# Kernel tuning notes

Hardware: AMD Instinct MI355X
Metric: run time of the kernel (lower is better)

Reference implementation:

```python
import jax, jax.numpy as jnp
import numpy as np

N_UNI = 32; N_G = 4; N_PPG = 8
MAX_D = 100.0; MIN_D = 0.5
SOM_SIGMA = 2.0; G_STD = 2.5
ORIG = jnp.array([-25.6, -25.6, -2.0], jnp.float32); VS = 0.4
NZ = 16; GW = 128; GL = 128; DIM = 128
H_IMG = 352; W_IMG = 1216

def pe(x):
    # positional encoding: num_freqs=6, include_input -> 3 + 36 = 39 dims
    f = 2.0 ** jnp.arange(6, dtype=x.dtype)
    xf = x[..., None] * f  # (...,3,6)
    s = x.shape[:-1]
    return jnp.concatenate([x, jnp.sin(xf).reshape(s + (18,)), jnp.cos(xf).reshape(s + (18,))], axis=-1)

def resnet_fc(z, x, P):
    # pixelNeRF-style ResnetFC with latent injection per block
    w_in, b_in, wz, bz, w0, b0, w1, b1, w_out, b_out = P
    h = x @ w_in + b_in
    for i in range(3):
        h = h + z @ wz[i] + bz[i]
        net = jax.nn.relu(h) @ w0[i] + b0[i]
        h = h + jax.nn.relu(net) @ w1[i] + b1[i]
    return jax.nn.relu(h) @ w_out + b_out

def trilinear(grid, pts):
    # grid: (NZ,GW,GL,DIM); pts: (N,3) lidar coords -> trilinear gather, 0 outside
    g = (pts - ORIG) / VS
    gx, gy, gz = g[:, 0], g[:, 1], g[:, 2]
    inb = (gx >= 0) & (gx <= GW - 1) & (gy >= 0) & (gy <= GL - 1) & (gz >= 0) & (gz <= NZ - 1)
    gx = jnp.clip(gx, 0.0, GW - 1.0); gy = jnp.clip(gy, 0.0, GL - 1.0); gz = jnp.clip(gz, 0.0, NZ - 1.0)
    x0 = jnp.clip(jnp.floor(gx).astype(jnp.int32), 0, GW - 2)
    y0 = jnp.clip(jnp.floor(gy).astype(jnp.int32), 0, GL - 2)
    z0 = jnp.clip(jnp.floor(gz).astype(jnp.int32), 0, NZ - 2)
    fx = gx - x0; fy = gy - y0; fz = gz - z0
    def c(zi, xi, yi, w):
        return grid[zi, xi, yi] * w[:, None]
    feat = (c(z0, x0, y0, (1 - fz) * (1 - fx) * (1 - fy)) + c(z0, x0, y0 + 1, (1 - fz) * (1 - fx) * fy)
            + c(z0, x0 + 1, y0, (1 - fz) * fx * (1 - fy)) + c(z0, x0 + 1, y0 + 1, (1 - fz) * fx * fy)
            + c(z0 + 1, x0, y0, fz * (1 - fx) * (1 - fy)) + c(z0 + 1, x0, y0 + 1, fz * (1 - fx) * fy)
            + c(z0 + 1, x0 + 1, y0, fz * fx * (1 - fy)) + c(z0 + 1, x0 + 1, y0 + 1, fz * fx * fy))
    return feat * inb[:, None].astype(feat.dtype)

def bilinear(img, uv):
    # img: (3,H,W); uv: (N,2) (u=col, v=row) -> (N,3)
    _, H, W = img.shape
    u = jnp.clip(uv[:, 0], 0.0, W - 1.0); v = jnp.clip(uv[:, 1], 0.0, H - 1.0)
    u0 = jnp.clip(jnp.floor(u).astype(jnp.int32), 0, W - 2)
    v0 = jnp.clip(jnp.floor(v).astype(jnp.int32), 0, H - 2)
    fu = u - u0; fv = v - v0
    g = lambda vi, ui: img[:, vi, ui]
    out = (g(v0, u0) * ((1 - fv) * (1 - fu)) + g(v0, u0 + 1) * ((1 - fv) * fu)
           + g(v0 + 1, u0) * (fv * (1 - fu)) + g(v0 + 1, u0 + 1) * (fv * fu))
    return out.T

def _forward(bev_feature, cam_K, img_source, img_target, T_source2infer, T_source2target,
             gaussian_noise, Pm, Pg, sampled_pixels):
    R = sampled_pixels.shape[0]
    # (B, C, W, L) -> (n_z, W, L, dim)
    vf = bev_feature[0].reshape(NZ, DIM, GW, GL).transpose(0, 2, 3, 1)
    inv_K = jnp.linalg.inv(cam_K)
    pix = sampled_pixels.astype(jnp.float32)
    homog = jnp.concatenate([pix, jnp.ones((R, 1), jnp.float32)], axis=1)
    dirs = homog @ inv_K.T
    unit = dirs / jnp.linalg.norm(dirs, axis=1, keepdims=True)  # (R,3) cam frame
    Rsi = T_source2infer[:3, :3]; tsi = T_source2infer[:3, 3]
    viewdir = unit @ Rsi.T  # lidar frame

    # --- predict per-ray gaussian means/stds at coarse segment centers ---
    base = (jnp.arange(N_G, dtype=jnp.float32) + 0.5) * (MAX_D / N_G)
    pg = (unit[:, None, :] * base[None, :, None]).reshape(-1, 3) @ Rsi.T + tsi
    fg = trilinear(vf, pg)
    vdg = jnp.broadcast_to(viewdir[:, None, :], (R, N_G, 3)).reshape(-1, 3)
    og = resnet_fc(fg, jnp.concatenate([pe(pg), vdg], axis=1), Pg)  # (R*N_G,2)
    means = jnp.clip(base[None, :] + og[:, 0].reshape(R, N_G), MIN_D, MAX_D)
    stds = G_STD * jax.nn.sigmoid(og[:, 1].reshape(R, N_G)) + 0.1

    # --- sample points: uniform + gaussian, sorted along ray ---
    d_g = jnp.clip(means[:, :, None] + stds[:, :, None] * gaussian_noise, MIN_D, MAX_D).reshape(R, N_G * N_PPG)
    d_u = jnp.broadcast_to(jnp.linspace(MIN_D, MAX_D, N_UNI, dtype=jnp.float32)[None, :], (R, N_UNI))
    d = jnp.sort(jnp.concatenate([d_u, d_g], axis=1), axis=1)  # (R,64)
    P = d.shape[1]
    pl = (unit[:, None, :] * d[..., None]).reshape(-1, 3) @ Rsi.T + tsi
    fl = trilinear(vf, pl)
    vd = jnp.broadcast_to(viewdir[:, None, :], (R, P, 3)).reshape(-1, 3)
    out = resnet_fc(fl, jnp.concatenate([pe(pl), vd], axis=1), Pm).reshape(R, P, 4)
    sigma = jax.nn.softplus(out[..., 0]); rgb = jax.nn.sigmoid(out[..., 1:])

    # --- volume rendering ---
    deltas = jnp.concatenate([d[:, 1:] - d[:, :-1], jnp.full((R, 1), 1e10, jnp.float32)], axis=1)
    alpha = 1.0 - jnp.exp(-sigma * deltas)
    trans = jnp.cumprod(1.0 - alpha + 1e-10, axis=1)
    trans = jnp.concatenate([jnp.ones((R, 1), jnp.float32), trans[:, :-1]], axis=1)
    w = alpha * trans
    depth = (w * d).sum(axis=1)          # (R,)
    color = (w[..., None] * rgb).sum(axis=1)  # (R,3)

    # --- losses ---
    diff = jnp.abs(means - jax.lax.stop_gradient(depth)[:, None])
    loss_dist = diff.min(axis=1)
    pdf = jnp.exp(-(d[:, None, :] - means[..., None]) ** 2 / (2.0 * stds[..., None] ** 2)) / (stds[..., None] * jnp.sqrt(2.0 * jnp.pi))
    loss_kl = (w * (-jnp.log(pdf.mean(axis=1) + 1e-6))).sum(axis=1)
    src = bilinear(img_source, pix)
    loss_color = jnp.abs(src - color)
    pcam = unit * depth[:, None]
    pt = pcam @ T_source2target[:3, :3].T + T_source2target[:3, 3]
    proj = pt @ cam_K.T
    uv = proj[:, :2] / jnp.clip(proj[:, 2:3], 1e-3)
    tgt = bilinear(img_target, uv)
    loss_reproj = jnp.abs(src - tgt)
    total = loss_reproj.mean() + loss_color.mean() + loss_kl.mean() + 0.01 * loss_dist.mean()
    return total

def setup_inputs() -> dict:
    key = jax.random.key(0)
    def rn(i, shape, s=1.0):
        return jax.random.normal(jax.random.fold_in(key, i), shape, jnp.float32) * s
    R = 4096
    inp = {}
    inp['bev_feature'] = rn(0, (1, NZ * DIM, GW, GL), 0.5)
    inp['cam_K'] = jnp.array([[720.0, 0.0, 608.0], [0.0, 720.0, 176.0], [0.0, 0.0, 1.0]], jnp.float32)
    inp['img_source'] = jax.random.uniform(jax.random.fold_in(key, 1), (3, H_IMG, W_IMG), jnp.float32)
    inp['img_target'] = jax.random.uniform(jax.random.fold_in(key, 2), (3, H_IMG, W_IMG), jnp.float32)
    Rcl = jnp.array([[0.0, 0.0, 1.0], [-1.0, 0.0, 0.0], [0.0, -1.0, 0.0]], jnp.float32)  # cam->lidar axes
    inp['T_source2infer'] = jnp.eye(4, dtype=jnp.float32).at[:3, :3].set(Rcl).at[:3, 3].set(jnp.array([0.5, 0.2, 0.1], jnp.float32))
    inp['T_source2target'] = jnp.eye(4, dtype=jnp.float32).at[0, 3].set(0.8).at[1, 3].set(0.05)
    inp['gaussian_noise'] = rn(3, (R, N_G, N_PPG))
    u = jax.random.randint(jax.random.fold_in(key, 4), (R,), 0, W_IMG)
    v = jax.random.randint(jax.random.fold_in(key, 5), (R,), 0, H_IMG)
    inp['sampled_pixels'] = jnp.stack([u, v], axis=1).astype(jnp.int32)
    for pfx, (i0, d_out) in {'m': (10, 4), 'g': (40, 2)}.items():
        inp[pfx + '_w_in'] = rn(i0, (42, 128), 0.05)
        inp[pfx + '_b_in'] = jnp.zeros((128,), jnp.float32)
        inp[pfx + '_wz'] = rn(i0 + 1, (3, 128, 128), 0.05)
        inp[pfx + '_bz'] = jnp.zeros((3, 128), jnp.float32)
        inp[pfx + '_w0'] = rn(i0 + 2, (3, 128, 128), 0.05)
        inp[pfx + '_b0'] = jnp.zeros((3, 128), jnp.float32)
        inp[pfx + '_w1'] = rn(i0 + 3, (3, 128, 128), 0.05)
        inp[pfx + '_b1'] = jnp.zeros((3, 128), jnp.float32)
        inp[pfx + '_w_out'] = rn(i0 + 4, (128, d_out), 0.05)
        inp[pfx + '_b_out'] = jnp.zeros((d_out,), jnp.float32)
    return inp

def reference(bev_feature, cam_K, img_source, img_target, T_source2infer, T_source2target,
              gaussian_noise, sampled_pixels,
              m_w_in, m_b_in, m_wz, m_bz, m_w0, m_b0, m_w1, m_b1, m_w_out, m_b_out,
              g_w_in, g_b_in, g_wz, g_bz, g_w0, g_b0, g_w1, g_b1, g_w_out, g_b_out):
    Pm = (m_w_in, m_b_in, m_wz, m_bz, m_w0, m_b0, m_w1, m_b1, m_w_out, m_b_out)
    Pg = (g_w_in, g_b_in, g_wz, g_bz, g_w0, g_b0, g_w1, g_b1, g_w_out, g_b_out)
    return _forward(bev_feature, cam_K, img_source, img_target, T_source2infer, T_source2target,
                    gaussian_noise, Pm, Pg, sampled_pixels)
```

## Files before the change

kernel.cpp:

```cpp
#include <hip/hip_runtime.h>

typedef __attribute__((ext_vector_type(8))) short short8;
typedef __attribute__((ext_vector_type(4))) float f32x4;
typedef unsigned short ushort_t;

#define WIMG 1216
#define HIMG 352

__device__ __forceinline__ float sigmoid_(float x){ return 1.f/(1.f+__expf(-x)); }
__device__ __forceinline__ float softplus_(float x){
  return fmaxf(x,0.f) + log1pf(__expf(-fabsf(x)));
}
__device__ __forceinline__ ushort_t f2b(float x){
  union { float f; unsigned u; } v; v.f = x;
  unsigned r = v.u + 0x7FFF + ((v.u >> 16) & 1);
  return (ushort_t)(r >> 16);
}
__device__ __forceinline__ ushort_t f2b_fast(float x){
  union { float f; unsigned u; } v; v.f = x;
  return (ushort_t)((v.u + 0x8000u) >> 16);
}
__device__ __forceinline__ unsigned pack2bf(float a, float b){
  union { float f; unsigned u; } va, vb; va.f = a; vb.f = b;
  return ((va.u + 0x8000u) >> 16) | ((vb.u + 0x8000u) & 0xFFFF0000u);
}
__device__ __forceinline__ float b2f(ushort_t b){
  union { unsigned u; float f; } v; v.u = ((unsigned)b) << 16;
  return v.f;
}
__device__ __forceinline__ float b2f_lo(unsigned u){
  union { unsigned u; float f; } v; v.u = u << 16; return v.f;
}
__device__ __forceinline__ float b2f_hi(unsigned u){
  union { unsigned u; float f; } v; v.u = u & 0xFFFF0000u; return v.f;
}

__global__ void k_pack(const float* __restrict__ w_in, const float* __restrict__ wz,
                       const float* __restrict__ w0, const float* __restrict__ w1,
                       const float* __restrict__ w_out, int outd,
                       ushort_t* __restrict__ pk){
  int id = blockIdx.x*256 + threadIdx.x;
  if (id >= 39*4096) return;
  int blk = id >> 12;
  int e = id & 4095;
  float val = 0.f;
  if (blk < 38) {
    int nt = e >> 9, lane = (e >> 3) & 63, j = e & 7;
    int kloc = (lane >> 4)*8 + j;
    int n = nt*16 + (lane & 15);
    if (blk < 2) {
      int k = blk*32 + kloc;
      val = (k < 42) ? w_in[k*128 + n] : 0.f;
    } else {
      int g = blk - 2;
      int i = g / 12, r = g % 12, m = r >> 2, ks = r & 3;
      int k = ks*32 + kloc;
      const float* src = (m==0 ? wz : (m==1 ? w0 : w1)) + i*16384;
      val = src[k*128 + n];
    }
  } else if (e < 2048) {
    int ks = e >> 9, lane = (e >> 3) & 63, j = e & 7;
    int k = ks*32 + (lane >> 4)*8 + j;
    int n = lane & 15;
    val = (n < outd) ? w_out[k*outd + n] : 0.f;
  }
  pk[id] = f2b(val);
}

__global__ void k_transpose(const float* __restrict__ src, ushort_t* __restrict__ dst){
  __shared__ float tile[32][33];
  int zx = blockIdx.z;
  int y0 = blockIdx.x * 32;
  int c0 = blockIdx.y * 32;
  int z = zx >> 7, x = zx & 127;
  const float* s = src + (size_t)z*2097152 + (size_t)x*128;
  for (int i = threadIdx.y; i < 32; i += 8)
    tile[i][threadIdx.x] = s[(size_t)(c0+i)*16384 + (size_t)(y0 + threadIdx.x)];
  __syncthreads();
  ushort_t* d = dst + ((size_t)zx*128 + y0)*128 + c0;
  int idx = threadIdx.y*32 + threadIdx.x;
  for (int it = 0; it < 2; ++it) {
    int lin = it*256 + idx;
    int y = lin >> 4, cp = lin & 15;
    unsigned o = pack2bf(tile[cp*2][y], tile[cp*2+1][y]);
    *(unsigned*)(d + (size_t)y*128 + cp*2) = o;
  }
}

__global__ void k_rayinit(const float* __restrict__ camK, const int* __restrict__ pix,
                          const float* __restrict__ Tsi,
                          float* __restrict__ unit, float* __restrict__ viewdir, int R){
  int r = blockIdx.x*blockDim.x + threadIdx.x;
  if (r >= R) return;
  float a=camK[0],b=camK[1],c=camK[2],d=camK[3],e=camK[4],f=camK[5],g=camK[6],h=camK[7],i=camK[8];
  float c00 = e*i-f*h, c01 = c*h-b*i, c02 = b*f-c*e;
  float c10 = f*g-d*i, c11 = a*i-c*g, c12 = c*d-a*f;
  float c20 = d*h-e*g, c21 = b*g-a*h, c22 = a*e-b*d;
  float det = a*c00 + b*c10 + c*c20;
  float id = 1.f/det;
  float u = (float)pix[2*r], v = (float)pix[2*r+1];
  float dx = (c00*u + c01*v + c02)*id;
  float dy = (c10*u + c11*v + c12)*id;
  float dz = (c20*u + c21*v + c22)*id;
  float n = sqrtf(dx*dx+dy*dy+dz*dz);
  dx/=n; dy/=n; dz/=n;
  unit[3*r]=dx; unit[3*r+1]=dy; unit[3*r+2]=dz;
  viewdir[3*r]   = Tsi[0]*dx + Tsi[1]*dy + Tsi[2]*dz;
  viewdir[3*r+1] = Tsi[4]*dx + Tsi[5]*dy + Tsi[6]*dz;
  viewdir[3*r+2] = Tsi[8]*dx + Tsi[9]*dy + Tsi[10]*dz;
}

template<int KS>
__device__ __forceinline__ void gemm_acc(const ushort_t* lds, int pitch,
                                         const ushort_t* __restrict__ pkB,
                                         f32x4 acc[4][2], int wave, int lane)
{
  int l15 = lane & 15, quad = lane >> 4;
  short8 b[2*KS];
  #pragma unroll
  for (int ks = 0; ks < KS; ++ks)
    #pragma unroll
    for (int ct = 0; ct < 2; ++ct)
      b[ks*2+ct] = *(const short8*)(pkB + (size_t)((ks*8 + wave*2 + ct)*64 + lane)*8);
  #pragma unroll
  for (int ks = 0; ks < KS; ++ks) {
    short8 a[4];
    #pragma unroll
    for (int rt = 0; rt < 4; ++rt)
      a[rt] = *(const short8*)(lds + (rt*16 + l15)*pitch + ks*32 + quad*8);
    #pragma unroll
    for (int rt = 0; rt < 4; ++rt)
      #pragma unroll
      for (int ct = 0; ct < 2; ++ct)
        acc[rt][ct] = __builtin_amdgcn_mfma_f32_16x16x32_bf16(a[rt], b[ks*2+ct], acc[rt][ct], 0,0,0);
  }
}

__device__ __forceinline__ void store_relu(ushort_t* buf, const f32x4 acc[4][2], int wave, int lane){
  int l15 = lane & 15, quad = lane >> 4;
  #pragma unroll
  for (int rt = 0; rt < 4; ++rt)
    #pragma unroll
    for (int ct = 0; ct < 2; ++ct) {
      int n = (wave*2+ct)*16 + l15;
      #pragma unroll
      for (int r = 0; r < 4; ++r) {
        int p = rt*16 + quad*4 + r;
        buf[p*136 + n] = f2b_fast(fmaxf(acc[rt][ct][r], 0.f));
      }
    }
}

template<int OUTD, int RAY_SHIFT>
__global__ __launch_bounds__(256, 4)
void k_fused(const ushort_t* __restrict__ vfh, const float* __restrict__ vf0, int mode,
             const float* __restrict__ unit, const float* __restrict__ viewdir,
             const float* __restrict__ Tsi, const float* __restrict__ dvals,
             const ushort_t* __restrict__ pk,
             const float* __restrict__ b_in, const float* __restrict__ bzv,
             const float* __restrict__ b0v, const float* __restrict__ b1v,
             const float* __restrict__ b_out,
             float* __restrict__ means, float* __restrict__ stds, float* __restrict__ outbuf)
{
  __shared__ int   sOff[64];
  __shared__ float sFx[64], sFy[64], sFz[64], sSc[64];
  __shared__ float sPx[64], sPy[64], sPz[64], sVx[64], sVy[64], sVz[64];
  __shared__ ushort_t zf[64*136];
  __shared__ ushort_t Wb[64*136];

  int tid = threadIdx.x;
  int qbase = blockIdx.x * 64;

  if (tid < 64) {
    int q = qbase + tid;
    int ray = q >> RAY_SHIFT;
    float t;
    if constexpr (OUTD == 2) t = ((float)(q & 3) + 0.5f) * 25.f;
    else                     t = dvals[q];
    float ux = unit[3*ray], uy = unit[3*ray+1], uz = unit[3*ray+2];
    float wx=ux*t, wy=uy*t, wz=uz*t;
    float px = Tsi[0]*wx + Tsi[1]*wy + Tsi[2]*wz + Tsi[3];
    float py = Tsi[4]*wx + Tsi[5]*wy + Tsi[6]*wz + Tsi[7];
    float pz = Tsi[8]*wx + Tsi[9]*wy + Tsi[10]*wz + Tsi[11];
    sPx[tid]=px; sPy[tid]=py; sPz[tid]=pz;
    sVx[tid]=viewdir[3*ray]; sVy[tid]=viewdir[3*ray+1]; sVz[tid]=viewdir[3*ray+2];
    float gx = (px + 25.6f)*2.5f;
    float gy = (py + 25.6f)*2.5f;
    float gz = (pz + 2.0f)*2.5f;
    bool inb = (gx>=0.f)&&(gx<=127.f)&&(gy>=0.f)&&(gy<=127.f)&&(gz>=0.f)&&(gz<=15.f);
    gx = fminf(fmaxf(gx,0.f),127.f);
    gy = fminf(fmaxf(gy,0.f),127.f);
    gz = fminf(fmaxf(gz,0.f),15.f);
    int x0 = min(max((int)floorf(gx),0),126);
    int y0 = min(max((int)floorf(gy),0),126);
    int z0 = min(max((int)floorf(gz),0),14);
    sFx[tid]=gx-(float)x0; sFy[tid]=gy-(float)y0; sFz[tid]=gz-(float)z0;
    sSc[tid]= inb ? 1.f : 0.f;
    sOff[tid] = mode ? (((z0*128 + x0)*128 + y0)*128)
                     : (z0*2097152 + x0*128 + y0);
  }
  __syncthreads();

  for (int it = 0; it < 16; ++it) {
    int lin = it*256 + tid;
    int p = lin >> 6, cp = lin & 63, c = cp*2;
    float fx=sFx[p], fy=sFy[p], fz=sFz[p], sc=sSc[p];
    float w000=(1.f-fz)*(1.f-fx)*(1.f-fy), w001=(1.f-fz)*(1.f-fx)*fy;
    float w010=(1.f-fz)*fx*(1.f-fy),       w011=(1.f-fz)*fx*fy;
    float w100=fz*(1.f-fx)*(1.f-fy),       w101=fz*(1.f-fx)*fy;
    float w110=fz*fx*(1.f-fy),             w111=fz*fx*fy;
    float r0, r1;
    if (mode) {
      const ushort_t* b = vfh + sOff[p] + c;
      unsigned v000 = *(const unsigned*)(b);
      unsigned v001 = *(const unsigned*)(b + 128);
      unsigned v010 = *(const unsigned*)(b + 16384);
      unsigned v011 = *(const unsigned*)(b + 16384 + 128);
      unsigned v100 = *(const unsigned*)(b + 2097152);
      unsigned v101 = *(const unsigned*)(b + 2097152 + 128);
      unsigned v110 = *(const unsigned*)(b + 2097152 + 16384);
      unsigned v111 = *(const unsigned*)(b + 2097152 + 16384 + 128);
      r0 = (w000*b2f_lo(v000) + w001*b2f_lo(v001) + w010*b2f_lo(v010) + w011*b2f_lo(v011)
          + w100*b2f_lo(v100) + w101*b2f_lo(v101) + w110*b2f_lo(v110) + w111*b2f_lo(v111)) * sc;
      r1 = (w000*b2f_hi(v000) + w001*b2f_hi(v001) + w010*b2f_hi(v010) + w011*b2f_hi(v011)
          + w100*b2f_hi(v100) + w101*b2f_hi(v101) + w110*b2f_hi(v110) + w111*b2f_hi(v111)) * sc;
    } else {
      const float* b = vf0 + sOff[p] + c*16384;
      r0 = (w000*b[0] + w001*b[1] + w010*b[128] + w011*b[129]
          + w100*b[2097152] + w101*b[2097153] + w110*b[2097280] + w111*b[2097281]) * sc;
      const float* b2 = b + 16384;
      r1 = (w000*b2[0] + w001*b2[1] + w010*b2[128] + w011*b2[129]
          + w100*b2[2097152] + w101*b2[2097153] + w110*b2[2097280] + w111*b2[2097281]) * sc;
    }
    *(unsigned*)(zf + p*136 + c) = pack2bf(r0, r1);
  }

  for (int it = 0; it < 16; ++it) {
    int lin = it*256 + tid;
    int p = lin >> 6, d = lin & 63;
    float val = 0.f;
    if (d < 3)      val = (d==0)?sPx[p]:((d==1)?sPy[p]:sPz[p]);
    else if (d < 39) {
      int s = d - 3; bool isSin = (s < 18); if (!isSin) s -= 18;
      int axis = s/6, fi = s%6;
      float base = (axis==0)?sPx[p]:((axis==1)?sPy[p]:sPz[p]);
      float arg = base * (float)(1 << fi);
      val = isSin ? __sinf(arg) : __cosf(arg);
    } else if (d < 42) {
      val = (d==39)?sVx[p]:((d==40)?sVy[p]:sVz[p]);
    }
    Wb[p*72 + d] = f2b_fast(val);
  }
  __syncthreads();

  int wave = tid >> 6, lane = tid & 63;
  int l15 = lane & 15, quad = lane >> 4;
  int n0 = (wave*2)*16 + l15;

  f32x4 h[4][2];
  {
    float bi0 = b_in[n0], bi1 = b_in[n0+16];
    #pragma unroll
    for (int rt = 0; rt < 4; ++rt) {
      h[rt][0] = (f32x4){bi0,bi0,bi0,bi0};
      h[rt][1] = (f32x4){bi1,bi1,bi1,bi1};
    }
  }
  gemm_acc<2>(Wb, 72, pk, h, wave, lane);

  const ushort_t* pkl = pk + 2*4096;
  #pragma unroll 1
  for (int i = 0; i < 3; ++i) {
    gemm_acc<4>(zf, 136, pkl + (size_t)(i*12)*4096, h, wave, lane);
    {
      float z0b = bzv[i*128 + n0], z1b = bzv[i*128 + n0 + 16];
      #pragma unroll
      for (int rt = 0; rt < 4; ++rt) { h[rt][0] += z0b; h[rt][1] += z1b; }
    }
    __syncthreads();
    store_relu(Wb, h, wave, lane);
    __syncthreads();
    f32x4 net[4][2];
    {
      float c0b = b0v[i*128 + n0], c1b = b0v[i*128 + n0 + 16];
      #pragma unroll
      for (int rt = 0; rt < 4; ++rt) {
        net[rt][0] = (f32x4){c0b,c0b,c0b,c0b};
        net[rt][1] = (f32x4){c1b,c1b,c1b,c1b};
      }
    }
    gemm_acc<4>(Wb, 136, pkl + (size_t)(i*12+4)*4096, net, wave, lane);
    __syncthreads();
    store_relu(Wb, net, wave, lane);
    __syncthreads();
    gemm_acc<4>(Wb, 136, pkl + (size_t)(i*12+8)*4096, h, wave, lane);
    {
      float o0b = b1v[i*128 + n0], o1b = b1v[i*128 + n0 + 16];
      #pragma unroll
      for (int rt = 0; rt < 4; ++rt) { h[rt][0] += o0b; h[rt][1] += o1b; }
    }
  }
  __syncthreads();
  store_relu(Wb, h, wave, lane);
  __syncthreads();

  {
    const ushort_t* pkw = pk + 38*4096;
    float bj = (l15 < OUTD) ? b_out[l15] : 0.f;
    f32x4 oa = (f32x4){bj,bj,bj,bj};
    #pragma unroll
    for (int ks = 0; ks < 4; ++ks) {
      short8 a = *(const short8*)(Wb + (wave*16 + l15)*136 + ks*32 + quad*8);
      short8 b = *(const short8*)(pkw + (size_t)(ks*64 + lane)*8);
      oa = __builtin_amdgcn_mfma_f32_16x16x32_bf16(a, b, oa, 0,0,0);
    }
    if (l15 < OUTD) {
      #pragma unroll
      for (int r = 0; r < 4; ++r) {
        int p = wave*16 + quad*4 + r;
        int q = qbase + p;
        if constexpr (OUTD == 4) {
          outbuf[(size_t)q*4 + l15] = oa[r];
        } else {
          int ray = q >> 2, g = q & 3;
          if (l15 == 0) means[ray*4+g] = fminf(fmaxf(((float)g + 0.5f)*25.f + oa[r], 0.5f), 100.f);
          else          stds[ray*4+g]  = 2.5f*sigmoid_(oa[r]) + 0.1f;
        }
      }
    }
  }
}

__global__ void k_sortd(const float* __restrict__ means, const float* __restrict__ stds,
                        const float* __restrict__ noise, float* __restrict__ dsort, int R){
  __shared__ float buf[4][64];
  int lr = threadIdx.x >> 6, p = threadIdx.x & 63;
  int ray = blockIdx.x*4 + lr;
  float val;
  if (p < 32) val = 0.5f + (float)p * (99.5f/31.f);
  else {
    int idx = p - 32, g = idx >> 3, s = idx & 7;
    float mu = means[ray*4+g], sd = stds[ray*4+g];
    val = fminf(fmaxf(mu + sd*noise[(ray*4+g)*8 + s], 0.5f), 100.f);
  }
  buf[lr][p] = val;
  __syncthreads();
  int rank = 0;
  for (int k = 0; k < 64; ++k) {
    float o = buf[lr][k];
    rank += (o < val) || (o == val && k < p);
  }
  dsort[ray*64 + rank] = val;
}

__device__ __forceinline__ void bilin3(const float* __restrict__ img, float u, float v, float* out){
  u = fminf(fmaxf(u, 0.f), (float)(WIMG-1));
  v = fminf(fmaxf(v, 0.f), (float)(HIMG-1));
  int u0 = min(max((int)floorf(u),0), WIMG-2);
  int v0 = min(max((int)floorf(v),0), HIMG-2);
  float fu = u - (float)u0, fv = v - (float)v0;
  float w00=(1.f-fv)*(1.f-fu), w01=(1.f-fv)*fu, w10=fv*(1.f-fu), w11=fv*fu;
  #pragma unroll
  for (int c = 0; c < 3; ++c) {
    const float* b = img + (size_t)c*(HIMG*WIMG) + (size_t)v0*WIMG + u0;
    out[c] = w00*b[0] + w01*b[1] + w10*b[WIMG] + w11*b[WIMG+1];
  }
}

__global__ void k_render(const float* __restrict__ outbuf, const float* __restrict__ dsort,
                         const float* __restrict__ means, const float* __restrict__ stds,
                         const float* __restrict__ unit,
                         const float* __restrict__ img_src, const float* __restrict__ img_tgt,
                         const int* __restrict__ pix, const float* __restrict__ camK,
                         const float* __restrict__ Tst, float* __restrict__ rayloss, int R){
  int gid = blockIdx.x*blockDim.x + threadIdx.x;
  int r = gid >> 6, lane = gid & 63;
  if (r >= R) return;
  float d = dsort[(size_t)r*64 + lane];
  float dn = __shfl_down(d, 1);
  float delta = (lane < 63) ? (dn - d) : 1e10f;
  float4 o = *(const float4*)(outbuf + (size_t)r*256 + lane*4);
  float sig = softplus_(o.x);
  float alpha = 1.f - __expf(-sig*delta);
  float om = 1.f - alpha + 1e-10f;
  float prod = om;
  #pragma unroll
  for (int off = 1; off < 64; off <<= 1) {
    float v = __shfl_up(prod, off);
    if (lane >= off) prod *= v;
  }
  float texc = __shfl_up(prod, 1);
  if (lane == 0) texc = 1.f;
  float w = alpha * texc;
  float m0=means[r*4],m1=means[r*4+1],m2=means[r*4+2],m3=means[r*4+3];
  float s0=stds[r*4], s1=stds[r*4+1], s2=stds[r*4+2], s3=stds[r*4+3];
  float t0=(d-m0)/s0, t1=(d-m1)/s1, t2=(d-m2)/s2, t3=(d-m3)/s3;
  float pm = 0.25f*0.3989422804014327f*(__expf(-0.5f*t0*t0)/s0 + __expf(-0.5f*t1*t1)/s1
                                      + __expf(-0.5f*t2*t2)/s2 + __expf(-0.5f*t3*t3)/s3);
  float kl  = w * (-__logf(pm + 1e-6f));
  float dep = w * d;
  float c0 = w * sigmoid_(o.y);
  float c1 = w * sigmoid_(o.z);
  float c2 = w * sigmoid_(o.w);
  #pragma unroll
  for (int off = 32; off; off >>= 1) {
    dep += __shfl_xor(dep, off);
    c0  += __shfl_xor(c0, off);
    c1  += __shfl_xor(c1, off);
    c2  += __shfl_xor(c2, off);
    kl  += __shfl_xor(kl, off);
  }
  if (lane == 0) {
    float ld = fminf(fminf(fabsf(m0-dep),fabsf(m1-dep)), fminf(fabsf(m2-dep),fabsf(m3-dep)));
    float src[3], tgt[3];
    float u = (float)pix[2*r], v = (float)pix[2*r+1];
    bilin3(img_src, u, v, src);
    float ux=unit[3*r],uy=unit[3*r+1],uz=unit[3*r+2];
    float pcx=ux*dep, pcy=uy*dep, pcz=uz*dep;
    float ptx = Tst[0]*pcx + Tst[1]*pcy + Tst[2]*pcz + Tst[3];
    float pty = Tst[4]*pcx + Tst[5]*pcy + Tst[6]*pcz + Tst[7];
    float ptz = Tst[8]*pcx + Tst[9]*pcy + Tst[10]*pcz + Tst[11];
    float prx = camK[0]*ptx + camK[1]*pty + camK[2]*ptz;
    float pry = camK[3]*ptx + camK[4]*pty + camK[5]*ptz;
    float prz = camK[6]*ptx + camK[7]*pty + camK[8]*ptz;
    prz = fmaxf(prz, 0.001f);
    bilin3(img_tgt, prx/prz, pry/prz, tgt);
    float lrepr = fabsf(src[0]-tgt[0])+fabsf(src[1]-tgt[1])+fabsf(src[2]-tgt[2]);
    float lcol  = fabsf(src[0]-c0)+fabsf(src[1]-c1)+fabsf(src[2]-c2);
    float invR = 1.f/(float)R;
    rayloss[r] = (lrepr + lcol) * (invR/3.f) + kl*invR + 0.01f*ld*invR;
  }
}

__global__ void k_reduce(const float* __restrict__ rayloss, float* __restrict__ out, int R){
  __shared__ float sm[256];
  float acc = 0.f;
  for (int i = threadIdx.x; i < R; i += 256) acc += rayloss[i];
  sm[threadIdx.x] = acc;
  __syncthreads();
  for (int s = 128; s > 0; s >>= 1) {
    if ((int)threadIdx.x < s) sm[threadIdx.x] += sm[threadIdx.x + s];
    __syncthreads();
  }
  if (threadIdx.x == 0) out[0] = sm[0];
}

extern "C" void kernel_launch(void* const* d_in, const int* in_sizes, int n_in,
                              void* d_out, int out_size, void* d_ws, size_t ws_size,
                              hipStream_t stream)
{
  const float* bev   = (const float*)d_in[0];
  const float* camK  = (const float*)d_in[1];
  const float* img_s = (const float*)d_in[2];
  const float* img_t = (const float*)d_in[3];
  const float* Tsi   = (const float*)d_in[4];
  const float* Tst   = (const float*)d_in[5];
  const float* noise = (const float*)d_in[6];
  const int*   pix   = (const int*)d_in[7];
  const float* m_w_in=(const float*)d_in[8];  const float* m_b_in=(const float*)d_in[9];
  const float* m_wz  =(const float*)d_in[10]; const float* m_bz  =(const float*)d_in[11];
  const float* m_w0  =(const float*)d_in[12]; const float* m_b0  =(const float*)d_in[13];
  const float* m_w1  =(const float*)d_in[14]; const float* m_b1  =(const float*)d_in[15];
  const float* m_wo  =(const float*)d_in[16]; const float* m_bo  =(const float*)d_in[17];
  const float* g_w_in=(const float*)d_in[18]; const float* g_b_in=(const float*)d_in[19];
  const float* g_wz  =(const float*)d_in[20]; const float* g_bz  =(const float*)d_in[21];
  const float* g_w0  =(const float*)d_in[22]; const float* g_b0  =(const float*)d_in[23];
  const float* g_w1  =(const float*)d_in[24]; const float* g_b1  =(const float*)d_in[25];
  const float* g_wo  =(const float*)d_in[26]; const float* g_bo  =(const float*)d_in[27];

  int R = in_sizes[7] / 2;
  float* ws = (float*)d_ws;
  size_t off = 0;
  float* unitb = ws + off; off += (size_t)R*3;
  float* vdirb = ws + off; off += (size_t)R*3;
  float* means = ws + off; off += (size_t)R*4;
  float* stds  = ws + off; off += (size_t)R*4;
  float* dsort = ws + off; off += (size_t)R*64;
  float* outbf = ws + off; off += (size_t)R*256;
  float* rlos  = ws + off; off += (size_t)R;
  ushort_t* pkM = (ushort_t*)(ws + off);
  ushort_t* pkG = pkM + 39*4096;
  off += 39*4096 + 64;
  off = (off + 63) & ~(size_t)63;
  ushort_t* vfh = (ushort_t*)(ws + off);
  size_t need = off*4ull + (size_t)16*128*128*128*2ull;
  int mode = (ws_size >= need) ? 1 : 0;

  k_pack<<<624,256,0,stream>>>(m_w_in, m_wz, m_w0, m_w1, m_wo, 4, pkM);
  k_pack<<<624,256,0,stream>>>(g_w_in, g_wz, g_w0, g_w1, g_wo, 2, pkG);
  if (mode) {
    dim3 g(4,4,2048), b(32,8);
    k_transpose<<<g,b,0,stream>>>(bev, vfh);
  }
  k_rayinit<<<(R+255)/256,256,0,stream>>>(camK,pix,Tsi,unitb,vdirb,R);
  k_fused<2,2><<<R/16,256,0,stream>>>(vfh,bev,mode,unitb,vdirb,Tsi,nullptr,pkG,
      g_b_in,g_bz,g_b0,g_b1,g_bo, means,stds,nullptr);
  k_sortd<<<R/4,256,0,stream>>>(means,stds,noise,dsort,R);
  k_fused<4,6><<<R,256,0,stream>>>(vfh,bev,mode,unitb,vdirb,Tsi,dsort,pkM,
      m_b_in,m_bz,m_b0,m_b1,m_bo, nullptr,nullptr,outbf);
  k_render<<<R/4,256,0,stream>>>(outbf,dsort,means,stds,unitb,img_s,img_t,pix,camK,Tst,rlos,R);
  k_reduce<<<1,256,0,stream>>>(rlos,(float*)d_out,R);
}
```

Baseline: 483.1 us.

## Transpose MFMA operands, vectorize trilinear gather, and precompute interpolation weights

The MLP GEMMs now put weights in the A operand and activations in B, so each lane's accumulator holds four consecutive channels. ReLU stores become packed 8-byte LDS writes and bias loads become vector loads. The trilinear gather now reads 8 bf16 channels per 16-byte load using per-point weights computed once into shared memory. The transpose kernel uses nontemporal accesses and truncating bf16 conversion, which changes rounding slightly compared with round-to-nearest.

```diff
diff --git a/kernel.cpp b/kernel.cpp
--- a/kernel.cpp
+++ b/kernel.cpp
@@ -20,13 +20,9 @@
   union { float f; unsigned u; } v; v.f = x;
   return (ushort_t)((v.u + 0x8000u) >> 16);
 }
-__device__ __forceinline__ unsigned pack2bf(float a, float b){
+__device__ __forceinline__ unsigned pack_trunc(float a, float b){
   union { float f; unsigned u; } va, vb; va.f = a; vb.f = b;
-  return ((va.u + 0x8000u) >> 16) | ((vb.u + 0x8000u) & 0xFFFF0000u);
-}
-__device__ __forceinline__ float b2f(ushort_t b){
-  union { unsigned u; float f; } v; v.u = ((unsigned)b) << 16;
-  return v.f;
+  return (va.u >> 16) | (vb.u & 0xFFFF0000u);
 }
 __device__ __forceinline__ float b2f_lo(unsigned u){
   union { unsigned u; float f; } v; v.u = u << 16; return v.f;
@@ -75,15 +71,15 @@
   int z = zx >> 7, x = zx & 127;
   const float* s = src + (size_t)z*2097152 + (size_t)x*128;
   for (int i = threadIdx.y; i < 32; i += 8)
-    tile[i][threadIdx.x] = s[(size_t)(c0+i)*16384 + (size_t)(y0 + threadIdx.x)];
+    tile[i][threadIdx.x] = __builtin_nontemporal_load(s + (size_t)(c0+i)*16384 + (size_t)(y0 + threadIdx.x));
   __syncthreads();
   ushort_t* d = dst + ((size_t)zx*128 + y0)*128 + c0;
   int idx = threadIdx.y*32 + threadIdx.x;
   for (int it = 0; it < 2; ++it) {
     int lin = it*256 + idx;
     int y = lin >> 4, cp = lin & 15;
-    unsigned o = pack2bf(tile[cp*2][y], tile[cp*2+1][y]);
-    *(unsigned*)(d + (size_t)y*128 + cp*2) = o;
+    unsigned o = pack_trunc(tile[cp*2][y], tile[cp*2+1][y]);
+    __builtin_nontemporal_store(o, (unsigned*)(d + (size_t)y*128 + cp*2));
   }
 }
 
@@ -111,43 +107,43 @@
 }
 
 template<int KS>
-__device__ __forceinline__ void gemm_acc(const ushort_t* lds, int pitch,
-                                         const ushort_t* __restrict__ pkB,
-                                         f32x4 acc[4][2], int wave, int lane)
+__device__ __forceinline__ void gemm_accT(const ushort_t* lds, int pitch,
+                                          const ushort_t* __restrict__ pkW,
+                                          f32x4 acc[2][4], int wave, int lane)
 {
   int l15 = lane & 15, quad = lane >> 4;
-  short8 b[2*KS];
+  short8 w[KS][2];
   #pragma unroll
   for (int ks = 0; ks < KS; ++ks)
     #pragma unroll
     for (int ct = 0; ct < 2; ++ct)
-      b[ks*2+ct] = *(const short8*)(pkB + (size_t)((ks*8 + wave*2 + ct)*64 + lane)*8);
+      w[ks][ct] = *(const short8*)(pkW + (size_t)((ks*8 + wave*2 + ct)*64 + lane)*8);
   #pragma unroll
   for (int ks = 0; ks < KS; ++ks) {
-    short8 a[4];
+    short8 b[4];
     #pragma unroll
-    for (int rt = 0; rt < 4; ++rt)
-      a[rt] = *(const short8*)(lds + (rt*16 + l15)*pitch + ks*32 + quad*8);
+    for (int nt = 0; nt < 4; ++nt)
+      b[nt] = *(const short8*)(lds + (nt*16 + l15)*pitch + ks*32 + quad*8);
     #pragma unroll
-    for (int rt = 0; rt < 4; ++rt)
+    for (int ct = 0; ct < 2; ++ct)
       #pragma unroll
-      for (int ct = 0; ct < 2; ++ct)
-        acc[rt][ct] = __builtin_amdgcn_mfma_f32_16x16x32_bf16(a[rt], b[ks*2+ct], acc[rt][ct], 0,0,0);
-  }
-}
-
-__device__ __forceinline__ void store_relu(ushort_t* buf, const f32x4 acc[4][2], int wave, int lane){
+      for (int nt = 0; nt < 4; ++nt)
+        acc[ct][nt] = __builtin_amdgcn_mfma_f32_16x16x32_bf16(w[ks][ct], b[nt], acc[ct][nt], 0,0,0);
+  }
+}
+
+__device__ __forceinline__ void store_reluT(ushort_t* buf, const f32x4 acc[2][4], int wave, int lane){
   int l15 = lane & 15, quad = lane >> 4;
   #pragma unroll
-  for (int rt = 0; rt < 4; ++rt)
+  for (int ct = 0; ct < 2; ++ct)
     #pragma unroll
-    for (int ct = 0; ct < 2; ++ct) {
-      int n = (wave*2+ct)*16 + l15;
-      #pragma unroll
-      for (int r = 0; r < 4; ++r) {
-        int p = rt*16 + quad*4 + r;
-        buf[p*136 + n] = f2b_fast(fmaxf(acc[rt][ct][r], 0.f));
-      }
+    for (int nt = 0; nt < 4; ++nt) {
+      float r0 = fmaxf(acc[ct][nt][0], 0.f);
+      float r1 = fmaxf(acc[ct][nt][1], 0.f);
+      float r2 = fmaxf(acc[ct][nt][2], 0.f);
+      float r3 = fmaxf(acc[ct][nt][3], 0.f);
+      uint2 o; o.x = pack_trunc(r0, r1); o.y = pack_trunc(r2, r3);
+      *(uint2*)(buf + (nt*16 + l15)*136 + (wave*2+ct)*16 + quad*4) = o;
     }
 }
 
@@ -163,7 +159,7 @@
              float* __restrict__ means, float* __restrict__ stds, float* __restrict__ outbuf)
 {
   __shared__ int   sOff[64];
-  __shared__ float sFx[64], sFy[64], sFz[64], sSc[64];
+  __shared__ float sW[64][8];
   __shared__ float sPx[64], sPy[64], sPz[64], sVx[64], sVy[64], sVz[64];
   __shared__ ushort_t zf[64*136];
   __shared__ ushort_t Wb[64*136];
@@ -194,45 +190,57 @@
     int x0 = min(max((int)floorf(gx),0),126);
     int y0 = min(max((int)floorf(gy),0),126);
     int z0 = min(max((int)floorf(gz),0),14);
-    sFx[tid]=gx-(float)x0; sFy[tid]=gy-(float)y0; sFz[tid]=gz-(float)z0;
-    sSc[tid]= inb ? 1.f : 0.f;
+    float fx = gx-(float)x0, fy = gy-(float)y0, fz = gz-(float)z0;
+    float sc = inb ? 1.f : 0.f;
+    float ax0 = 1.f-fx, ay0 = 1.f-fy;
+    float az0 = (1.f-fz)*sc, az1 = fz*sc;
+    float q00 = ax0*ay0, q01 = ax0*fy, q10 = fx*ay0, q11 = fx*fy;
+    sW[tid][0] = az0*q00; sW[tid][1] = az0*q01; sW[tid][2] = az0*q10; sW[tid][3] = az0*q11;
+    sW[tid][4] = az1*q00; sW[tid][5] = az1*q01; sW[tid][6] = az1*q10; sW[tid][7] = az1*q11;
     sOff[tid] = mode ? (((z0*128 + x0)*128 + y0)*128)
                      : (z0*2097152 + x0*128 + y0);
   }
   __syncthreads();
 
-  for (int it = 0; it < 16; ++it) {
+  for (int it = 0; it < 4; ++it) {
     int lin = it*256 + tid;
-    int p = lin >> 6, cp = lin & 63, c = cp*2;
-    float fx=sFx[p], fy=sFy[p], fz=sFz[p], sc=sSc[p];
-    float w000=(1.f-fz)*(1.f-fx)*(1.f-fy), w001=(1.f-fz)*(1.f-fx)*fy;
-    float w010=(1.f-fz)*fx*(1.f-fy),       w011=(1.f-fz)*fx*fy;
-    float w100=fz*(1.f-fx)*(1.f-fy),       w101=fz*(1.f-fx)*fy;
-    float w110=fz*fx*(1.f-fy),             w111=fz*fx*fy;
-    float r0, r1;
+    int p = lin >> 4, cb = lin & 15;
+    float4 wA = *(const float4*)&sW[p][0];
+    float4 wB = *(const float4*)&sW[p][4];
+    float r0=0,r1=0,r2=0,r3=0,r4=0,r5=0,r6=0,r7=0;
     if (mode) {
-      const ushort_t* b = vfh + sOff[p] + c;
-      unsigned v000 = *(const unsigned*)(b);
-      unsigned v001 = *(const unsigned*)(b + 128);
-      unsigned v010 = *(const unsigned*)(b + 16384);
-      unsigned v011 = *(const unsigned*)(b + 16384 + 128);
-      unsigned v100 = *(const unsigned*)(b + 2097152);
-      unsigned v101 = *(const unsigned*)(b + 2097152 + 128);
-      unsigned v110 = *(const unsigned*)(b + 2097152 + 16384);
-      unsigned v111 = *(const unsigned*)(b + 2097152 + 16384 + 128);
-      r0 = (w000*b2f_lo(v000) + w001*b2f_lo(v001) + w010*b2f_lo(v010) + w011*b2f_lo(v011)
-          + w100*b2f_lo(v100) + w101*b2f_lo(v101) + w110*b2f_lo(v110) + w111*b2f_lo(v111)) * sc;
-      r1 = (w000*b2f_hi(v000) + w001*b2f_hi(v001) + w010*b2f_hi(v010) + w011*b2f_hi(v011)
-          + w100*b2f_hi(v100) + w101*b2f_hi(v101) + w110*b2f_hi(v110) + w111*b2f_hi(v111)) * sc;
+      const ushort_t* b = vfh + sOff[p] + cb*8;
+      uint4 v;
+      #define ACC8(PTR, W) \
+        v = *(const uint4*)(PTR); \
+        r0 += (W)*b2f_lo(v.x); r1 += (W)*b2f_hi(v.x); \
+        r2 += (W)*b2f_lo(v.y); r3 += (W)*b2f_hi(v.y); \
+        r4 += (W)*b2f_lo(v.z); r5 += (W)*b2f_hi(v.z); \
+        r6 += (W)*b2f_lo(v.w); r7 += (W)*b2f_hi(v.w);
+      ACC8(b,                     wA.x)
+      ACC8(b + 128,               wA.y)
+      ACC8(b + 16384,             wA.z)
+      ACC8(b + 16384 + 128,       wA.w)
+      ACC8(b + 2097152,           wB.x)
+      ACC8(b + 2097152 + 128,     wB.y)
+      ACC8(b + 2097152 + 16384,   wB.z)
+      ACC8(b + 2097152 + 16512,   wB.w)
+      #undef ACC8
     } else {
-      const float* b = vf0 + sOff[p] + c*16384;
-      r0 = (w000*b[0] + w001*b[1] + w010*b[128] + w011*b[129]
-          + w100*b[2097152] + w101*b[2097153] + w110*b[2097280] + w111*b[2097281]) * sc;
-      const float* b2 = b + 16384;
-      r1 = (w000*b2[0] + w001*b2[1] + w010*b2[128] + w011*b2[129]
-          + w100*b2[2097152] + w101*b2[2097153] + w110*b2[2097280] + w111*b2[2097281]) * sc;
-    }
-    *(unsigned*)(zf + p*136 + c) = pack2bf(r0, r1);
+      const float* bsrc = vf0 + sOff[p];
+      float rr[8];
+      #pragma unroll
+      for (int k = 0; k < 8; ++k) {
+        const float* bc = bsrc + (size_t)(cb*8 + k)*16384;
+        rr[k] = wA.x*bc[0] + wA.y*bc[1] + wA.z*bc[128] + wA.w*bc[129]
+              + wB.x*bc[2097152] + wB.y*bc[2097153] + wB.z*bc[2097280] + wB.w*bc[2097281];
+      }
+      r0=rr[0]; r1=rr[1]; r2=rr[2]; r3=rr[3]; r4=rr[4]; r5=rr[5]; r6=rr[6]; r7=rr[7];
+    }
+    uint4 o;
+    o.x = pack_trunc(r0, r1); o.y = pack_trunc(r2, r3);
+    o.z = pack_trunc(r4, r5); o.w = pack_trunc(r6, r7);
+    *(uint4*)(zf + p*136 + cb*8) = o;
   }
 
   for (int it = 0; it < 16; ++it) {
@@ -255,77 +263,71 @@
 
   int wave = tid >> 6, lane = tid & 63;
   int l15 = lane & 15, quad = lane >> 4;
-  int n0 = (wave*2)*16 + l15;
-
-  f32x4 h[4][2];
+  int cbase = wave*32 + quad*4;
+
+  f32x4 h[2][4];
   {
-    float bi0 = b_in[n0], bi1 = b_in[n0+16];
+    f32x4 bi0 = *(const f32x4*)(b_in + cbase);
+    f32x4 bi1 = *(const f32x4*)(b_in + cbase + 16);
     #pragma unroll
-    for (int rt = 0; rt < 4; ++rt) {
-      h[rt][0] = (f32x4){bi0,bi0,bi0,bi0};
-      h[rt][1] = (f32x4){bi1,bi1,bi1,bi1};
-    }
-  }
-  gemm_acc<2>(Wb, 72, pk, h, wave, lane);
+    for (int nt = 0; nt < 4; ++nt) { h[0][nt] = bi0; h[1][nt] = bi1; }
+  }
+  gemm_accT<2>(Wb, 72, pk, h, wave, lane);
 
   const ushort_t* pkl = pk + 2*4096;
   #pragma unroll 1
   for (int i = 0; i < 3; ++i) {
-    gemm_acc<4>(zf, 136, pkl + (size_t)(i*12)*4096, h, wave, lane);
+    gemm_accT<4>(zf, 136, pkl + (size_t)(i*12)*4096, h, wave, lane);
     {
-      float z0b = bzv[i*128 + n0], z1b = bzv[i*128 + n0 + 16];
+      f32x4 bz0 = *(const f32x4*)(bzv + i*128 + cbase);
+      f32x4 bz1 = *(const f32x4*)(bzv + i*128 + cbase + 16);
       #pragma unroll
-      for (int rt = 0; rt < 4; ++rt) { h[rt][0] += z0b; h[rt][1] += z1b; }
+      for (int nt = 0; nt < 4; ++nt) { h[0][nt] += bz0; h[1][nt] += bz1; }
     }
     __syncthreads();
-    store_relu(Wb, h, wave, lane);
+    store_reluT(Wb, h, wave, lane);
     __syncthreads();
-    f32x4 net[4][2];
+    f32x4 net[2][4];
     {
-      float c0b = b0v[i*128 + n0], c1b = b0v[i*128 + n0 + 16];
+      f32x4 c0b = *(const f32x4*)(b0v + i*128 + cbase);
+      f32x4 c1b = *(const f32x4*)(b0v + i*128 + cbase + 16);
       #pragma unroll
-      for (int rt = 0; rt < 4; ++rt) {
-        net[rt][0] = (f32x4){c0b,c0b,c0b,c0b};
-        net[rt][1] = (f32x4){c1b,c1b,c1b,c1b};
-      }
-    }
-    gemm_acc<4>(Wb, 136, pkl + (size_t)(i*12+4)*4096, net, wave, lane);
+      for (int nt = 0; nt < 4; ++nt) { net[0][nt] = c0b; net[1][nt] = c1b; }
+    }
+    gemm_accT<4>(Wb, 136, pkl + (size_t)(i*12+4)*4096, net, wave, lane);
     __syncthreads();
-    store_relu(Wb, net, wave, lane);
+    store_reluT(Wb, net, wave, lane);
     __syncthreads();
-    gemm_acc<4>(Wb, 136, pkl + (size_t)(i*12+8)*4096, h, wave, lane);
+    gemm_accT<4>(Wb, 136, pkl + (size_t)(i*12+8)*4096, h, wave, lane);
     {
-      float o0b = b1v[i*128 + n0], o1b = b1v[i*128 + n0 + 16];
+      f32x4 o0b = *(const f32x4*)(b1v + i*128 + cbase);
+      f32x4 o1b = *(const f32x4*)(b1v + i*128 + cbase + 16);
       #pragma unroll
-      for (int rt = 0; rt < 4; ++rt) { h[rt][0] += o0b; h[rt][1] += o1b; }
-    }
-  }
-  __syncthreads();
-  store_relu(Wb, h, wave, lane);
+      for (int nt = 0; nt < 4; ++nt) { h[0][nt] += o0b; h[1][nt] += o1b; }
+    }
+  }
+  __syncthreads();
+  store_reluT(Wb, h, wave, lane);
   __syncthreads();
 
   {
     const ushort_t* pkw = pk + 38*4096;
-    float bj = (l15 < OUTD) ? b_out[l15] : 0.f;
-    f32x4 oa = (f32x4){bj,bj,bj,bj};
+    f32x4 oa = (f32x4){0.f,0.f,0.f,0.f};
     #pragma unroll
     for (int ks = 0; ks < 4; ++ks) {
-      short8 a = *(const short8*)(Wb + (wave*16 + l15)*136 + ks*32 + quad*8);
-      short8 b = *(const short8*)(pkw + (size_t)(ks*64 + lane)*8);
-      oa = __builtin_amdgcn_mfma_f32_16x16x32_bf16(a, b, oa, 0,0,0);
-    }
-    if (l15 < OUTD) {
-      #pragma unroll
-      for (int r = 0; r < 4; ++r) {
-        int p = wave*16 + quad*4 + r;
-        int q = qbase + p;
-        if constexpr (OUTD == 4) {
-          outbuf[(size_t)q*4 + l15] = oa[r];
-        } else {
-          int ray = q >> 2, g = q & 3;
-          if (l15 == 0) means[ray*4+g] = fminf(fmaxf(((float)g + 0.5f)*25.f + oa[r], 0.5f), 100.f);
-          else          stds[ray*4+g]  = 2.5f*sigmoid_(oa[r]) + 0.1f;
-        }
+      short8 w = *(const short8*)(pkw + (size_t)(ks*64 + lane)*8);
+      short8 b = *(const short8*)(Wb + (wave*16 + l15)*136 + ks*32 + quad*8);
+      oa = __builtin_amdgcn_mfma_f32_16x16x32_bf16(w, b, oa, 0,0,0);
+    }
+    if (quad == 0) {
+      int q = qbase + wave*16 + l15;
+      if constexpr (OUTD == 4) {
+        float4 o = { oa[0] + b_out[0], oa[1] + b_out[1], oa[2] + b_out[2], oa[3] + b_out[3] };
+        *(float4*)(outbuf + (size_t)q*4) = o;
+      } else {
+        int g = q & 3;
+        means[q] = fminf(fmaxf(((float)g + 0.5f)*25.f + oa[0] + b_out[0], 0.5f), 100.f);
+        stds[q]  = 2.5f*sigmoid_(oa[1] + b_out[1]) + 0.1f;
       }
     }
   }
```

Result: faster. 458.8 us (-5.0%).
